# Performance work log

Measured on AMD Instinct MI355X. Metric: run time of the kernel, lower is better.

The kernel has to match this reference:

```python
import jax, jax.numpy as jnp
import numpy as np

LBDA = 0.1  # softmin temperature used by OTAM_cum_dist in this repo family


def otam_cum_dist(dists):
    # dists: [Q, S, Tq, Ts] frame-to-frame distances
    Q, S, Tq, Ts = dists.shape
    d = jnp.pad(dists, ((0, 0), (0, 0), (0, 0), (1, 1)))  # zero-pad support axis -> width W = Ts + 2
    W = Ts + 2
    # top row: cum[0, m] = d[0, m] + cum[0, m-1]  (plain cumulative sum, cum[0,0]=0 since d[...,0]=0)
    row0 = jnp.cumsum(d[:, :, 0, :], axis=-1)  # [Q, S, W]

    # column m gets the extra term prev_row[m] only at the first (m=1) and last (m=W-1) columns
    incl = jnp.zeros(W - 1, dtype=bool).at[0].set(True).at[-1].set(True)

    def row_step(prev_row, d_row):
        # prev_row, d_row: [Q, S, W]; move column axis to front for the scan
        d_cols = jnp.moveaxis(d_row[:, :, 1:], -1, 0)        # d[l, m],    m = 1..W-1  -> [W-1, Q, S]
        prev_mm1 = jnp.moveaxis(prev_row[:, :, :-1], -1, 0)  # prev[m-1]
        prev_m = jnp.moveaxis(prev_row[:, :, 1:], -1, 0)     # prev[m]

        def col_step(carry, xs):
            # carry = cum[l, m-1] (starts at cum[l,0] = 0)
            d_m, p_mm1, p_m, inc = xs
            t3 = jnp.where(inc, -p_m / LBDA, -jnp.inf)
            neg = jnp.stack([-p_mm1 / LBDA, -carry / LBDA, t3])  # [3, Q, S]
            val = d_m - LBDA * jax.nn.logsumexp(neg, axis=0)     # softmin recurrence
            return val, val

        _, cols = jax.lax.scan(col_step, jnp.zeros((Q, S), d.dtype),
                               (d_cols, prev_mm1, prev_m, incl))
        new_row = jnp.concatenate([jnp.zeros((Q, S, 1), d.dtype),
                                   jnp.moveaxis(cols, 0, -1)], axis=-1)
        return new_row, None

    d_rows = jnp.moveaxis(d[:, :, 1:, :], 2, 0)  # [Tq-1, Q, S, W]
    last_row, _ = jax.lax.scan(row_step, row0, d_rows)
    return last_row[:, :, -1]  # cum_dists[..., -1, -1] -> [Q, S]


def setup_inputs() -> dict:
    key = jax.random.key(0)
    similarity = jax.random.uniform(key, (2048, 128, 16, 16), dtype=jnp.float32)
    return {"similarity": similarity}


def reference(similarity):
    distance = 1.0 - similarity
    votes = otam_cum_dist(distance) + otam_cum_dist(jnp.swapaxes(distance, -1, -2))
    return -(0.5 * votes)  # [query count, support count]
```

## Files before the change

kernel.cpp:

```cpp
#include <hip/hip_runtime.h>


#define K2   14.4269504088896340736f
#define LL2  0.069314718055994530942f

__device__ __forceinline__ float softmin2(float a, float b) {
    float mn = fminf(a, b);
    float t  = __builtin_amdgcn_exp2f(-K2 * fabsf(a - b));
    return mn - LL2 * __builtin_amdgcn_logf(1.0f + t);
}

__device__ __forceinline__ float softmin3(float a, float b, float c) {
    float mn = fminf(fminf(a, b), c);
    float s = __builtin_amdgcn_exp2f(-K2 * (a - mn))
            + __builtin_amdgcn_exp2f(-K2 * (b - mn))
            + __builtin_amdgcn_exp2f(-K2 * (c - mn));
    return mn - LL2 * __builtin_amdgcn_logf(s);
}

__device__ __forceinline__ void dp_row(float* R, const float* dr) {
    float diag = R[0];
    float oldR = R[1];
    R[1] = dr[0] + softmin3(diag, R[0], oldR);
    diag = oldR;
#pragma unroll
    for (int m = 2; m <= 16; ++m) {
        float o = R[m];
        R[m] = dr[m - 1] + softmin2(diag, R[m - 1]);
        diag = o;
    }
    R[17] = softmin3(diag, R[16], R[17]);
}

__device__ __forceinline__ void dp_col(float* C, const float* dr) {
    float diag2 = C[0];
    C[0] = C[0] + dr[0];
#pragma unroll
    for (int l = 1; l < 16; ++l) {
        float o = C[l];
        C[l] = dr[l] + softmin2(diag2, o);
        diag2 = o;
    }
}


__global__ __launch_bounds__(256, 2)
void otam_fused_kernel(const float* __restrict__ sim, float* __restrict__ out) {
    const int t  = threadIdx.x & 63;
    const int wv = threadIdx.x >> 6;
    const int pair0 = blockIdx.x * 256 + wv * 64;

    __shared__ float lds_all[4 * 1024];
    float* lds = lds_all + (wv << 10);

    const int u = t >> 2;
    const int q = t & 3;
    const float* gsrc = sim + (((size_t)(pair0 + u)) << 8) + (q << 2);
    float* wbase = lds + ((u * 4 + (q ^ ((t >> 3) & 3))) << 2);

    float R[18], C[16], dr[16];
    float4 A[4], B[4];

#define LOADN(buf, r)                                                              \
    _Pragma("unroll")                                                              \
    for (int i = 0; i < 4; ++i)                                                    \
        buf[i] = *reinterpret_cast<const float4*>(gsrc + (r) * 16 + i * 4096);

#define WRITEC(buf)                                                                \
    _Pragma("unroll")                                                              \
    for (int i = 0; i < 4; ++i) {                                                  \
        float4 w;                                                                  \
        w.x = 1.0f - buf[i].x; w.y = 1.0f - buf[i].y;                              \
        w.z = 1.0f - buf[i].z; w.w = 1.0f - buf[i].w;                              \
        *reinterpret_cast<float4*>(wbase + i * 256) = w;                           \
    }

#define READR()                                                                    \
    _Pragma("unroll")                                                              \
    for (int j = 0; j < 4; ++j) {                                                  \
        float4 v = *reinterpret_cast<const float4*>(                               \
            lds + t * 16 + ((j ^ ((t >> 1) & 3)) << 2));                           \
        dr[j * 4 + 0] = v.x; dr[j * 4 + 1] = v.y;                                  \
        dr[j * 4 + 2] = v.z; dr[j * 4 + 3] = v.w;                                  \
    }

    LOADN(A, 0);
    LOADN(B, 1);
    WRITEC(A);
    READR();
    R[0] = 0.0f;
#pragma unroll
    for (int m = 1; m <= 16; ++m) R[m] = R[m - 1] + dr[m - 1];
    R[17] = R[16];
    C[0] = dr[0];
#pragma unroll
    for (int l = 1; l < 16; ++l)
        C[l] = dr[l] + softmin3(0.0f, 0.0f, C[l - 1]);

#pragma unroll
    for (int r = 1; r < 16; ++r) {
        if (r & 1) {
            if (r < 15) LOADN(A, r + 1);
            WRITEC(B);
        } else {
            if (r < 15) LOADN(B, r + 1);
            WRITEC(A);
        }
        READR();
        dp_row(R, dr);
        dp_col(C, dr);
    }

    {
        float diag2 = C[0];
#pragma unroll
        for (int l = 1; l < 16; ++l) {
            float o = C[l];
            C[l] = softmin3(diag2, o, C[l - 1]);
            diag2 = o;
        }
    }

    out[pair0 + t] = -0.5f * (R[17] + C[15]);
#undef LOADN
#undef WRITEC
#undef READR
}

extern "C" void kernel_launch(void* const* d_in, const int* in_sizes, int n_in,
                              void* d_out, int out_size, void* d_ws, size_t ws_size,
                              hipStream_t stream) {
    const float* sim = (const float*)d_in[0];
    float* out = (float*)d_out;
    int npairs = in_sizes[0] >> 8;
    int grid = npairs >> 8;
    otam_fused_kernel<<<grid, 256, 0, stream>>>(sim, out);
}
```

Before: 66.59 us.

## Load two rows per chunk with 32-byte-per-thread staging through larger LDS

The global-to-LDS staging now moves two rows (32 floats) per pair per chunk, using 8 lanes per pair and an XOR swizzle over 8 slots. LDS per wave doubles, and the 16-row loop becomes an 8-iteration rolled loop that processes two DP rows per chunk. The aim is wider, more contiguous global loads and fewer load/write phases. In exchange it drops the double buffering, so loads for the next chunk are only issued partway through each iteration, and the rolled loop may cost register or scheduling freedom.

```diff
diff --git a/kernel.cpp b/kernel.cpp
--- a/kernel.cpp
+++ b/kernel.cpp
@@ -43,51 +43,51 @@
     }
 }
 
-
 __global__ __launch_bounds__(256, 2)
 void otam_fused_kernel(const float* __restrict__ sim, float* __restrict__ out) {
     const int t  = threadIdx.x & 63;
     const int wv = threadIdx.x >> 6;
     const int pair0 = blockIdx.x * 256 + wv * 64;
 
-    __shared__ float lds_all[4 * 1024];
-    float* lds = lds_all + (wv << 10);
+    __shared__ float lds_all[4 * 2048];
+    float* lds = lds_all + (wv << 11);
 
-    const int u = t >> 2;
-    const int q = t & 3;
-    const float* gsrc = sim + (((size_t)(pair0 + u)) << 8) + (q << 2);
-    float* wbase = lds + ((u * 4 + (q ^ ((t >> 3) & 3))) << 2);
+    const int u = t >> 3;
+    const int c = t & 7;
+
+    const float* gbase = sim + (((size_t)(pair0 + u)) << 8) + (c << 2);
+    float* wbase = lds + ((u * 8 + (c ^ u)) << 2);
 
     float R[18], C[16], dr[16];
-    float4 A[4], B[4];
+    float4 ld[8];
 
-#define LOADN(buf, r)                                                              \
+#define LOADN(cc)                                                                  \
     _Pragma("unroll")                                                              \
-    for (int i = 0; i < 4; ++i)                                                    \
-        buf[i] = *reinterpret_cast<const float4*>(gsrc + (r) * 16 + i * 4096);
+    for (int i = 0; i < 8; ++i)                                                    \
+        ld[i] = *reinterpret_cast<const float4*>(gbase + i * 2048 + (cc) * 32);
 
-#define WRITEC(buf)                                                                \
+#define WRITEC()                                                                   \
     _Pragma("unroll")                                                              \
-    for (int i = 0; i < 4; ++i) {                                                  \
+    for (int i = 0; i < 8; ++i) {                                                  \
         float4 w;                                                                  \
-        w.x = 1.0f - buf[i].x; w.y = 1.0f - buf[i].y;                              \
-        w.z = 1.0f - buf[i].z; w.w = 1.0f - buf[i].w;                              \
+        w.x = 1.0f - ld[i].x; w.y = 1.0f - ld[i].y;                                \
+        w.z = 1.0f - ld[i].z; w.w = 1.0f - ld[i].w;                                \
         *reinterpret_cast<float4*>(wbase + i * 256) = w;                           \
     }
 
-#define READR()                                                                    \
+#define READR(rr)                                                                  \
     _Pragma("unroll")                                                              \
-    for (int j = 0; j < 4; ++j) {                                                  \
+    for (int k = 0; k < 4; ++k) {                                                  \
         float4 v = *reinterpret_cast<const float4*>(                               \
-            lds + t * 16 + ((j ^ ((t >> 1) & 3)) << 2));                           \
-        dr[j * 4 + 0] = v.x; dr[j * 4 + 1] = v.y;                                  \
-        dr[j * 4 + 2] = v.z; dr[j * 4 + 3] = v.w;                                  \
+            lds + t * 32 + ((((rr) * 4 + k) ^ c) << 2));                           \
+        dr[k * 4 + 0] = v.x; dr[k * 4 + 1] = v.y;                                  \
+        dr[k * 4 + 2] = v.z; dr[k * 4 + 3] = v.w;                                  \
     }
 
-    LOADN(A, 0);
-    LOADN(B, 1);
-    WRITEC(A);
-    READR();
+    LOADN(0);
+    WRITEC();
+
+    READR(0);
     R[0] = 0.0f;
 #pragma unroll
     for (int m = 1; m <= 16; ++m) R[m] = R[m - 1] + dr[m - 1];
@@ -97,16 +97,19 @@
     for (int l = 1; l < 16; ++l)
         C[l] = dr[l] + softmin3(0.0f, 0.0f, C[l - 1]);
 
-#pragma unroll
-    for (int r = 1; r < 16; ++r) {
-        if (r & 1) {
-            if (r < 15) LOADN(A, r + 1);
-            WRITEC(B);
-        } else {
-            if (r < 15) LOADN(B, r + 1);
-            WRITEC(A);
-        }
-        READR();
+    LOADN(1);
+
+    READR(1);
+    dp_row(R, dr);
+    dp_col(C, dr);
+
+    for (int cc = 1; cc < 8; ++cc) {
+        WRITEC();
+        READR(0);
+        dp_row(R, dr);
+        dp_col(C, dr);
+        if (cc < 7) LOADN(cc + 1);
+        READR(1);
         dp_row(R, dr);
         dp_col(C, dr);
     }
```

Result: faster. 53.36 us, median of 2 (-19.9%).
